# Performance work log

Measured on AMD Instinct MI355X. Metric: run time of the kernel, lower is better.

Reference implementation:

```python
import jax, jax.numpy as jnp
import numpy as np

B, L, D_NODE, D_EDGE, H = 4, 256, 256, 128, 8
DK = D_NODE // H        # 32, per-head node dim
DE = D_EDGE // H        # 16, per-head edge dim
NEG_SLOPE = 0.2

# Static index maps replicating the torch loop indexing (including its j-1 off-by-one / wraparound bug)
_GIDX = np.arange(L - 1)[None, :] + (np.arange(L - 1)[None, :] >= np.arange(L)[:, None])  # [L, L-1]: j-values visited for row i (j != i, in order)
_PIDX = (np.arange(L) - 1) % (L - 1)   # [L]: torch uses attention_probs[:, j-1] for every j != i
_II = np.arange(L)[:, None]            # [L, 1]


def lrelu(x):
    return jnp.where(x >= 0, x, NEG_SLOPE * x)


def setup_inputs() -> dict:
    key = jax.random.key(0)
    ks = jax.random.split(key, 19)
    w = lambda k, s, sc=0.05: jax.random.normal(k, s, jnp.float32) * sc
    return dict(
        node=w(ks[0], (B, L, D_NODE), 1.0),
        edge=w(ks[1], (B, L, L, D_EDGE), 1.0),
        Wn_w=w(ks[2], (D_NODE, D_NODE)), Wn_b=w(ks[3], (D_NODE,)),
        Wh_w=w(ks[4], (DK, DK)), Wh_b=w(ks[5], (DK,)),
        We_w=w(ks[6], (D_EDGE, D_EDGE)), We_b=w(ks[7], (D_EDGE,)),
        Wn2_w=w(ks[8], (D_NODE, D_NODE)), Wn2_b=w(ks[9], (D_NODE,)),
        We2_w=w(ks[10], (D_EDGE, D_EDGE)), We2_b=w(ks[11], (D_EDGE,)),
        attn_w=w(ks[12], (2 * DK + DE,)),                  # attn_linear (no bias), input order [hi, hj, eij]
        edge_w=w(ks[13], (DE + 2 * DK, DE)), edge_b=w(ks[14], (DE,)),  # edge_linear, input order [eij, hi, hj]
        out_n_w=w(ks[15], (D_NODE, D_NODE)), out_n_b=w(ks[16], (D_NODE,)),
        out_e_w=w(ks[17], (D_EDGE, D_EDGE)), out_e_b=w(ks[18], (D_EDGE,)),
    )


def reference(node, edge, Wn_w, Wn_b, Wh_w, Wh_b, We_w, We_b, Wn2_w, Wn2_b,
              We2_w, We2_b, attn_w, edge_w, edge_b, out_n_w, out_n_b, out_e_w, out_e_b):
    node_p = (node @ Wn_w + Wn_b).reshape(B, L, H, DK)
    edge_p = (edge @ We_w + We_b).reshape(B, L, L, H, DE)

    # ---- node update (all heads at once) ----
    wq, wk, we = attn_w[:DK], attn_w[DK:2 * DK], attn_w[2 * DK:]
    si = jnp.einsum('bihd,d->bih', node_p, wq)
    sj = jnp.einsum('bjhd,d->bjh', node_p, wk)
    se = jnp.einsum('bijhd,d->bijh', edge_p, we)
    scores = si[:, :, None, :] + sj[:, None, :, :] + se          # [B,L,L,H], score(i,j)
    sc = scores[:, _II, _GIDX, :]                                 # [B,L,L-1,H]: j != i, loop order
    probs = jax.nn.softmax(lrelu(sc), axis=2)                     # softmax over the L-1 neighbors
    probs_pair = probs[:, :, _PIDX, :]                            # [B,L,L,H]: replicate probs[:, j-1]
    mask = (1.0 - jnp.eye(L, dtype=node.dtype))[None, :, :, None]
    Whh = jnp.einsum('bjhd,de->bjhe', node_p, Wh_w) + Wh_b        # Wh(hj), bias inside the sum
    agg = jnp.einsum('bijh,bjhe->bihe', probs_pair * mask, Whh)
    node_h = (node_p + lrelu(agg)).reshape(B, L, D_NODE)          # concat heads == reshape
    new_node = node_h @ out_n_w + out_n_b

    # ---- edge update ----
    node_p2 = (new_node @ Wn2_w + Wn2_b).reshape(B, L, H, DK)
    edge_p2 = (edge @ We2_w + We2_b).reshape(B, L, L, H, DE)
    w_e, w_i, w_j = edge_w[:DE], edge_w[DE:DE + DK], edge_w[DE + DK:]
    e_new = (jnp.einsum('bijhd,de->bijhe', edge_p2, w_e)
             + jnp.einsum('bihd,de->bihe', node_p2, w_i)[:, :, None]
             + jnp.einsum('bjhd,de->bjhe', node_p2, w_j)[:, None]
             + edge_b)
    e_new = e_new * mask[..., None]                               # diagonal stays zero (zeros_like init)
    new_edge = e_new.reshape(B, L, L, D_EDGE) @ out_e_w + out_e_b
    return new_node, new_edge
```

## Files before the change

kernel.cpp:

```cpp
#include <hip/hip_runtime.h>

#define Bb 4
#define Ll 256
#define NEG 0.2f

typedef __attribute__((ext_vector_type(8))) short short8;
typedef __attribute__((ext_vector_type(4))) float f32x4;
typedef __attribute__((ext_vector_type(4))) unsigned uint4v;

__device__ __forceinline__ float lrelu(float x) { return x >= 0.f ? x : NEG * x; }

__device__ __forceinline__ short f2bf(float x) {
  unsigned u = __builtin_bit_cast(unsigned, x);
  unsigned r = (u + 0x7FFFu + ((u >> 16) & 1u)) >> 16;
  return (short)r;
}

__device__ __forceinline__ unsigned pack2bf(float e, float o) {
  unsigned ue = __builtin_bit_cast(unsigned, e);
  unsigned uo = __builtin_bit_cast(unsigned, o);
  return ((ue + 0x8000u) >> 16) | ((uo + 0x8000u) & 0xFFFF0000u);
}

__global__ void prep_kernel(const float* We_w, const float* We_b, const float* attn_w,
                            const float* We2_w, const float* We2_b, const float* edge_w,
                            const float* edge_b, const float* out_e_w, const float* out_e_b,
                            short* Vbf, float* chg, float* c0g, short* Gt) {
  int blk = blockIdx.x;
  int t = threadIdx.x;
  if (blk < 128) {
    __shared__ float m2[128];
    int c = blk;
    int h = t >> 4, e = t & 15;
    float s = 0.f;
    for (int d = 0; d < 16; ++d) s += We2_w[c * 128 + h * 16 + d] * edge_w[d * 16 + e];
    m2[t] = s;
    __syncthreads();
    float g = 0.f;
    for (int f = 0; f < 128; ++f) g += m2[f] * out_e_w[f * 128 + t];
    Gt[t * 128 + c] = f2bf(g);
  } else {
    __shared__ float b2e[128];
    const float* we = attn_w + 64;
    for (int idx = t; idx < 1024; idx += 128) {
      int c = idx >> 3, h = idx & 7;
      float s = 0.f;
      for (int d = 0; d < 16; ++d) s += We_w[c * 128 + h * 16 + d] * we[d];
      Vbf[h * 128 + c] = f2bf(s);
      Vbf[(h + 8) * 128 + c] = 0;
    }
    if (t < 8) {
      float s = 0.f;
      for (int d = 0; d < 16; ++d) s += We_b[t * 16 + d] * we[d];
      chg[t] = s;
    }
    {
      int h = t >> 4, e = t & 15;
      float s = 0.f;
      for (int d = 0; d < 16; ++d) s += We2_b[h * 16 + d] * edge_w[d * 16 + e];
      b2e[t] = s + edge_b[e];
    }
    __syncthreads();
    float s = out_e_b[t];
    for (int f = 0; f < 128; ++f) s += b2e[f] * out_e_w[f * 128 + t];
    c0g[t] = s;
  }
}

template <bool WE>
__global__ __launch_bounds__(256) void pass_a(const float* __restrict__ edge,
                                              const short* __restrict__ Vbf,
                                              const float* __restrict__ chg,
                                              short* __restrict__ ebf,
                                              float* __restrict__ seg) {
  int t = threadIdx.x;
  int l = t & 63, w = t >> 6;
  int lc = l & 15, lq = l >> 4;
  long slab = blockIdx.x;
  const float* ebase = edge + slab * 32768;

  short8 vb[4];
#pragma unroll
  for (int ks = 0; ks < 4; ++ks) vb[ks] = *(const short8*)(Vbf + lc * 128 + ks * 32 + lq * 8);

  f32x4 acc[4];
#pragma unroll
  for (int mf = 0; mf < 4; ++mf) acc[mf] = (f32x4){0.f, 0.f, 0.f, 0.f};

#pragma unroll
  for (int mf = 0; mf < 4; ++mf) {
    int row = w * 64 + mf * 16 + lc;
    const float* ap = ebase + row * 128 + lq * 8;
    float4 f[8];
#pragma unroll
    for (int ks = 0; ks < 4; ++ks) {
      f[2 * ks] = *(const float4*)(ap + ks * 32);
      f[2 * ks + 1] = *(const float4*)(ap + ks * 32 + 4);
    }
#pragma unroll
    for (int ks = 0; ks < 4; ++ks) {
      uint4v u;
      u.x = pack2bf(f[2 * ks].x, f[2 * ks].y);
      u.y = pack2bf(f[2 * ks].z, f[2 * ks].w);
      u.z = pack2bf(f[2 * ks + 1].x, f[2 * ks + 1].y);
      u.w = pack2bf(f[2 * ks + 1].z, f[2 * ks + 1].w);
      if constexpr (WE) *(uint4v*)(ebf + slab * 32768 + row * 128 + ks * 32 + lq * 8) = u;
      acc[mf] = __builtin_amdgcn_mfma_f32_16x16x32_bf16(vb[ks], __builtin_bit_cast(short8, u),
                                                        acc[mf], 0, 0, 0);
    }
  }
  if (lq < 2) {
    f32x4 chv = *(const f32x4*)(chg + lq * 4);
#pragma unroll
    for (int mf = 0; mf < 4; ++mf) {
      int row = w * 64 + mf * 16 + lc;
      f32x4 v = acc[mf] + chv;
      *(f32x4*)(seg + slab * 2048 + row * 8 + lq * 4) = v;
    }
  }
}

__global__ __launch_bounds__(256) void node_in_fused(
    const float* __restrict__ node, const float* __restrict__ Wn_w,
    const float* __restrict__ Wn_b, const float* __restrict__ Wh_w,
    const float* __restrict__ Wh_b, const float* __restrict__ attn_w,
    float* __restrict__ node_p, float* __restrict__ Whh, float* __restrict__ si,
    float* __restrict__ sj) {
  __shared__ float a[4][256];
  __shared__ float np[4][256];
  int t = threadIdx.x;
  int row0 = blockIdx.x * 4;
  for (int q = t; q < 1024; q += 256) a[q >> 8][q & 255] = node[(long)row0 * 256 + q];
  __syncthreads();
  float acc[4];
  float bvv = Wn_b[t];
#pragma unroll
  for (int r = 0; r < 4; ++r) acc[r] = bvv;
  for (int k = 0; k < 256; ++k) {
    float w = Wn_w[k * 256 + t];
#pragma unroll
    for (int r = 0; r < 4; ++r) acc[r] += a[r][k] * w;
  }
#pragma unroll
  for (int r = 0; r < 4; ++r) {
    node_p[(long)(row0 + r) * 256 + t] = acc[r];
    np[r][t] = acc[r];
  }
  __syncthreads();
  int h = t >> 5, e = t & 31;
  float wb2 = Wh_b[e];
#pragma unroll
  for (int r = 0; r < 4; ++r) {
    float s = wb2;
    for (int d = 0; d < 32; ++d) s += np[r][h * 32 + d] * Wh_w[d * 32 + e];
    Whh[(long)(row0 + r) * 256 + t] = s;
  }
  if (t < 64) {
    int r = t >> 4, idx = t & 15, hh = idx & 7;
    const float* w = attn_w + (idx < 8 ? 0 : 32);
    float s = 0.f;
    for (int d = 0; d < 32; ++d) s += np[r][hh * 32 + d] * w[d];
    ((idx < 8) ? si : sj)[(long)(row0 + r) * 8 + hh] = s;
  }
}

__global__ __launch_bounds__(256) void attn_fused(
    const float* __restrict__ node_p, const float* __restrict__ Whh,
    const float* __restrict__ si, const float* __restrict__ sj,
    const float* __restrict__ seg, float* __restrict__ node_h) {
  __shared__ float sjl[2048];
  __shared__ float sel[2048];
  __shared__ float pl[2048];
  __shared__ float sil[8];
  int t = threadIdx.x, bi = blockIdx.x;
  int b = bi >> 8, i = bi & 255;
  for (int q = t; q < 2048; q += 256) sjl[q] = sj[(long)b * 2048 + q];
  for (int q = t; q < 2048; q += 256) sel[q] = seg[(long)bi * 2048 + q];
  if (t < 8) sil[t] = si[(long)bi * 8 + t];
  __syncthreads();

  int g = t >> 5, l32 = t & 31;
  float sc[8];
  float mx = -1e30f;
#pragma unroll
  for (int m = 0; m < 8; ++m) {
    int k = l32 + 32 * m;
    float v = -1e30f;
    if (k < 255) {
      int jj = k + (k >= i ? 1 : 0);
      v = sil[g] + sjl[jj * 8 + g] + sel[jj * 8 + g];
      v = lrelu(v);
    }
    sc[m] = v;
    mx = fmaxf(mx, v);
  }
#pragma unroll
  for (int d = 16; d >= 1; d >>= 1) mx = fmaxf(mx, __shfl_xor(mx, d));
  float sum = 0.f;
#pragma unroll
  for (int m = 0; m < 8; ++m) {
    int k = l32 + 32 * m;
    float e = (k < 255) ? __expf(sc[m] - mx) : 0.f;
    sc[m] = e;
    sum += e;
  }
#pragma unroll
  for (int d = 16; d >= 1; d >>= 1) sum += __shfl_xor(sum, d);
  float inv = 1.f / sum;
#pragma unroll
  for (int m = 0; m < 8; ++m) {
    int k = l32 + 32 * m;
    if (k < 255) pl[k * 8 + g] = sc[m] * inv;
  }
  __syncthreads();

  int h = g;
  const float* wb = Whh + (long)b * 65536 + t;
  float acc0 = 0.f, acc1 = 0.f;
#pragma unroll 8
  for (int j = 0; j < 256; j += 2) {
    int k0 = (j == 0) ? 254 : (j - 1);
    int k1 = j;
    float w0 = (j == i) ? 0.f : pl[k0 * 8 + h];
    float w1 = (j + 1 == i) ? 0.f : pl[k1 * 8 + h];
    acc0 += w0 * wb[(long)j * 256];
    acc1 += w1 * wb[(long)(j + 1) * 256];
  }
  float acc = acc0 + acc1;
  float np = node_p[(long)bi * 256 + t];
  node_h[(long)bi * 256 + t] = np + lrelu(acc);
}

__global__ __launch_bounds__(256) void node_out_pq(
    const float* __restrict__ node_h, const float* __restrict__ out_n_w,
    const float* __restrict__ out_n_b, const float* __restrict__ Wn2_w,
    const float* __restrict__ Wn2_b, const float* __restrict__ edge_w,
    const float* __restrict__ out_e_w, float* __restrict__ out_node,
    float* __restrict__ Pg, float* __restrict__ Qg) {
  __shared__ float a[4][256];
  __shared__ float b2[4][256];
  __shared__ float ninj[4][256];
  int t = threadIdx.x;
  int row0 = blockIdx.x * 4;
  for (int q = t; q < 1024; q += 256) a[q >> 8][q & 255] = node_h[(long)row0 * 256 + q];
  __syncthreads();
  float acc[4];
  float bv1 = out_n_b[t];
#pragma unroll
  for (int r = 0; r < 4; ++r) acc[r] = bv1;
  for (int k = 0; k < 256; ++k) {
    float w = out_n_w[k * 256 + t];
#pragma unroll
    for (int r = 0; r < 4; ++r) acc[r] += a[r][k] * w;
  }
#pragma unroll
  for (int r = 0; r < 4; ++r) {
    out_node[(long)(row0 + r) * 256 + t] = acc[r];
    b2[r][t] = acc[r];
  }
  __syncthreads();
  float acc2[4];
  float bv2 = Wn2_b[t];
#pragma unroll
  for (int r = 0; r < 4; ++r) acc2[r] = bv2;
  for (int k = 0; k < 256; ++k) {
    float w = Wn2_w[k * 256 + t];
#pragma unroll
    for (int r = 0; r < 4; ++r) acc2[r] += b2[r][k] * w;
  }
#pragma unroll
  for (int r = 0; r < 4; ++r) a[r][t] = acc2[r];
  __syncthreads();
  {
    int f = t & 127, h = f >> 4, e = f & 15;
    const float* w = edge_w + 256 + (t >> 7) * 512;
#pragma unroll
    for (int r = 0; r < 4; ++r) {
      float s = 0.f;
      for (int d = 0; d < 32; ++d) s += a[r][h * 32 + d] * w[d * 16 + e];
      ninj[r][t] = s;
    }
  }
  __syncthreads();
  {
    int o = t & 127;
    int half = (t >> 7) * 128;
#pragma unroll
    for (int r = 0; r < 4; ++r) {
      float s = 0.f;
      const float* src = ninj[r] + half;
      for (int f = 0; f < 128; ++f) s += src[f] * out_e_w[f * 128 + o];
      ((t < 128) ? Pg : Qg)[(long)(row0 + r) * 128 + o] = s;
    }
  }
}

template <bool UE>
__global__ __launch_bounds__(256) void edge_out_kernel(
    const float* __restrict__ edge, const short* __restrict__ ebf,
    const short* __restrict__ Gt, const float* __restrict__ Pg,
    const float* __restrict__ Qg, const float* __restrict__ c0g,
    const float* __restrict__ oeb, float* __restrict__ out_edge) {
  int t = threadIdx.x;
  int l = t & 63, wid = t >> 6;
  int wm = wid >> 1, wn = wid & 1;
  int lc = l & 15, lq = l >> 4;

  long row0 = (long)blockIdx.x * 128;
  int b = (int)(row0 >> 16);
  int i = (int)((row0 >> 8) & 255);
  int j0 = (int)(row0 & 255);

  short8 bv[4][4];
#pragma unroll
  for (int ks = 0; ks < 4; ++ks)
#pragma unroll
    for (int nf = 0; nf < 4; ++nf)
      bv[ks][nf] = *(const short8*)(Gt + (wn * 64 + nf * 16 + lc) * 128 + ks * 32 + lq * 8);

  f32x4 acc[4][4];
#pragma unroll
  for (int mf = 0; mf < 4; ++mf)
#pragma unroll
    for (int nf = 0; nf < 4; ++nf) acc[mf][nf] = (f32x4){0.f, 0.f, 0.f, 0.f};

#pragma unroll
  for (int ks = 0; ks < 4; ++ks) {
    short8 av[4];
#pragma unroll
    for (int mf = 0; mf < 4; ++mf) {
      long row = row0 + wm * 64 + mf * 16 + lc;
      if constexpr (UE) {
        av[mf] = *(const short8*)(ebf + row * 128 + ks * 32 + lq * 8);
      } else {
        const float* ap = edge + row * 128 + ks * 32 + lq * 8;
        float4 f0 = *(const float4*)ap;
        float4 f1 = *(const float4*)(ap + 4);
        uint4v u;
        u.x = pack2bf(f0.x, f0.y);
        u.y = pack2bf(f0.z, f0.w);
        u.z = pack2bf(f1.x, f1.y);
        u.w = pack2bf(f1.z, f1.w);
        av[mf] = __builtin_bit_cast(short8, u);
      }
    }
#pragma unroll
    for (int mf = 0; mf < 4; ++mf)
#pragma unroll
      for (int nf = 0; nf < 4; ++nf)
        acc[mf][nf] =
            __builtin_amdgcn_mfma_f32_16x16x32_bf16(bv[ks][nf], av[mf], acc[mf][nf], 0, 0, 0);
  }

  f32x4 pc[4];
#pragma unroll
  for (int nf = 0; nf < 4; ++nf) {
    int cb = wn * 64 + nf * 16 + lq * 4;
    f32x4 p = *(const f32x4*)(Pg + ((long)(b * 256 + i)) * 128 + cb);
    f32x4 c0 = *(const f32x4*)(c0g + cb);
    pc[nf] = p + c0;
  }
#pragma unroll
  for (int mf = 0; mf < 4; ++mf) {
    int er = wm * 64 + mf * 16 + lc;
    int j = j0 + er;
    const float* Qrow = Qg + ((long)(b * 256 + j)) * 128;
    float* orow = out_edge + (row0 + er) * 128;
    if (j == i) {
#pragma unroll
      for (int nf = 0; nf < 4; ++nf) {
        int cb = wn * 64 + nf * 16 + lq * 4;
        *(f32x4*)(orow + cb) = *(const f32x4*)(oeb + cb);
      }
    } else {
#pragma unroll
      for (int nf = 0; nf < 4; ++nf) {
        int cb = wn * 64 + nf * 16 + lq * 4;
        f32x4 q4 = *(const f32x4*)(Qrow + cb);
        *(f32x4*)(orow + cb) = acc[mf][nf] + pc[nf] + q4;
      }
    }
  }
}

extern "C" void kernel_launch(void* const* d_in, const int* in_sizes, int n_in,
                              void* d_out, int out_size, void* d_ws, size_t ws_size,
                              hipStream_t stream) {
  const float* node = (const float*)d_in[0];
  const float* edge = (const float*)d_in[1];
  const float* Wn_w = (const float*)d_in[2];
  const float* Wn_b = (const float*)d_in[3];
  const float* Wh_w = (const float*)d_in[4];
  const float* Wh_b = (const float*)d_in[5];
  const float* We_w = (const float*)d_in[6];
  const float* We_b = (const float*)d_in[7];
  const float* Wn2_w = (const float*)d_in[8];
  const float* Wn2_b = (const float*)d_in[9];
  const float* We2_w = (const float*)d_in[10];
  const float* We2_b = (const float*)d_in[11];
  const float* attn_w = (const float*)d_in[12];
  const float* edge_w = (const float*)d_in[13];
  const float* edge_b = (const float*)d_in[14];
  const float* out_n_w = (const float*)d_in[15];
  const float* out_n_b = (const float*)d_in[16];
  const float* out_e_w = (const float*)d_in[17];
  const float* out_e_b = (const float*)d_in[18];

  float* out_node = (float*)d_out;
  float* out_edge = ((float*)d_out) + 262144;

  float* ws = (float*)d_ws;
  float* node_p = ws;
  float* Whh    = ws + 262144;
  float* node_h = ws + 524288;
  float* si     = ws + 786432;
  float* sjv    = ws + 794624;
  float* Pg     = ws + 802816;
  float* Qg     = ws + 933888;
  float* chg    = ws + 1064960;
  float* c0g    = ws + 1065088;
  short* Gt     = (short*)(ws + 1065216);
  short* Vbf    = (short*)(ws + 1073408);
  float* seg    = ws + 1074432;
  short* ebf    = (short*)(ws + 3171584);
  const bool big = ws_size >= (size_t)19948800 * 4;

  prep_kernel<<<129, 128, 0, stream>>>(We_w, We_b, attn_w, We2_w, We2_b, edge_w, edge_b,
                                       out_e_w, out_e_b, Vbf, chg, c0g, Gt);
  node_in_fused<<<256, 256, 0, stream>>>(node, Wn_w, Wn_b, Wh_w, Wh_b, attn_w, node_p, Whh,
                                         si, sjv);
  if (big)
    pass_a<true><<<1024, 256, 0, stream>>>(edge, Vbf, chg, ebf, seg);
  else
    pass_a<false><<<1024, 256, 0, stream>>>(edge, Vbf, chg, ebf, seg);
  attn_fused<<<1024, 256, 0, stream>>>(node_p, Whh, si, sjv, seg, node_h);
  node_out_pq<<<256, 256, 0, stream>>>(node_h, out_n_w, out_n_b, Wn2_w, Wn2_b, edge_w,
                                       out_e_w, out_node, Pg, Qg);
  if (big)
    edge_out_kernel<true><<<2048, 256, 0, stream>>>(edge, ebf, Gt, Pg, Qg, c0g, out_e_b,
                                                    out_edge);
  else
    edge_out_kernel<false><<<2048, 256, 0, stream>>>(edge, ebf, Gt, Pg, Qg, c0g, out_e_b,
                                                     out_edge);
}
```

Baseline: 193.5 us.

## Fuse edge-score MFMA into attention kernel and split bf16 packing pass

The pass_a kernel is removed. Its per-row edge score MFMA now runs inside attn_fused, which writes results straight to shared memory, so the seg buffer no longer makes a global round-trip. A separate streaming pack_kernel converts edge to bf16 for later reuse, and attn_fused reads that bf16 copy, which halves the edge bytes it reads. The edge-output stores become nontemporal to reduce cache pollution. In exchange there is an extra kernel launch, and attn_fused takes on more register and latency load.

```diff
diff --git a/kernel.cpp b/kernel.cpp
--- a/kernel.cpp
+++ b/kernel.cpp
@@ -67,56 +67,21 @@
   }
 }
 
-template <bool WE>
-__global__ __launch_bounds__(256) void pass_a(const float* __restrict__ edge,
-                                              const short* __restrict__ Vbf,
-                                              const float* __restrict__ chg,
-                                              short* __restrict__ ebf,
-                                              float* __restrict__ seg) {
-  int t = threadIdx.x;
-  int l = t & 63, w = t >> 6;
-  int lc = l & 15, lq = l >> 4;
-  long slab = blockIdx.x;
-  const float* ebase = edge + slab * 32768;
-
-  short8 vb[4];
-#pragma unroll
-  for (int ks = 0; ks < 4; ++ks) vb[ks] = *(const short8*)(Vbf + lc * 128 + ks * 32 + lq * 8);
-
-  f32x4 acc[4];
-#pragma unroll
-  for (int mf = 0; mf < 4; ++mf) acc[mf] = (f32x4){0.f, 0.f, 0.f, 0.f};
-
-#pragma unroll
-  for (int mf = 0; mf < 4; ++mf) {
-    int row = w * 64 + mf * 16 + lc;
-    const float* ap = ebase + row * 128 + lq * 8;
-    float4 f[8];
-#pragma unroll
-    for (int ks = 0; ks < 4; ++ks) {
-      f[2 * ks] = *(const float4*)(ap + ks * 32);
-      f[2 * ks + 1] = *(const float4*)(ap + ks * 32 + 4);
-    }
-#pragma unroll
-    for (int ks = 0; ks < 4; ++ks) {
-      uint4v u;
-      u.x = pack2bf(f[2 * ks].x, f[2 * ks].y);
-      u.y = pack2bf(f[2 * ks].z, f[2 * ks].w);
-      u.z = pack2bf(f[2 * ks + 1].x, f[2 * ks + 1].y);
-      u.w = pack2bf(f[2 * ks + 1].z, f[2 * ks + 1].w);
-      if constexpr (WE) *(uint4v*)(ebf + slab * 32768 + row * 128 + ks * 32 + lq * 8) = u;
-      acc[mf] = __builtin_amdgcn_mfma_f32_16x16x32_bf16(vb[ks], __builtin_bit_cast(short8, u),
-                                                        acc[mf], 0, 0, 0);
-    }
-  }
-  if (lq < 2) {
-    f32x4 chv = *(const f32x4*)(chg + lq * 4);
-#pragma unroll
-    for (int mf = 0; mf < 4; ++mf) {
-      int row = w * 64 + mf * 16 + lc;
-      f32x4 v = acc[mf] + chv;
-      *(f32x4*)(seg + slab * 2048 + row * 8 + lq * 4) = v;
-    }
+__global__ __launch_bounds__(256) void pack_kernel(const float* __restrict__ edge,
+                                                   short* __restrict__ ebf) {
+  long base = (long)blockIdx.x * 256 + threadIdx.x;
+#pragma unroll
+  for (int it = 0; it < 8; ++it) {
+    long g = base + (long)it * 524288;
+    const float4* src = reinterpret_cast<const float4*>(edge + g * 8);
+    float4 f0 = src[0];
+    float4 f1 = src[1];
+    uint4v u;
+    u.x = pack2bf(f0.x, f0.y);
+    u.y = pack2bf(f0.z, f0.w);
+    u.z = pack2bf(f1.x, f1.y);
+    u.w = pack2bf(f1.z, f1.w);
+    *(uint4v*)(ebf + g * 8) = u;
   }
 }
 
@@ -164,10 +129,13 @@
   }
 }
 
+template <bool UE>
 __global__ __launch_bounds__(256) void attn_fused(
     const float* __restrict__ node_p, const float* __restrict__ Whh,
     const float* __restrict__ si, const float* __restrict__ sj,
-    const float* __restrict__ seg, float* __restrict__ node_h) {
+    const short* __restrict__ ebf, const float* __restrict__ edge,
+    const short* __restrict__ Vbf, const float* __restrict__ chg,
+    float* __restrict__ node_h) {
   __shared__ float sjl[2048];
   __shared__ float sel[2048];
   __shared__ float pl[2048];
@@ -175,8 +143,49 @@
   int t = threadIdx.x, bi = blockIdx.x;
   int b = bi >> 8, i = bi & 255;
   for (int q = t; q < 2048; q += 256) sjl[q] = sj[(long)b * 2048 + q];
-  for (int q = t; q < 2048; q += 256) sel[q] = seg[(long)bi * 2048 + q];
   if (t < 8) sil[t] = si[(long)bi * 8 + t];
+
+  {
+    int l = t & 63, w = t >> 6;
+    int lc = l & 15, lq = l >> 4;
+    short8 vb[4];
+#pragma unroll
+    for (int ks = 0; ks < 4; ++ks) vb[ks] = *(const short8*)(Vbf + lc * 128 + ks * 32 + lq * 8);
+    f32x4 acc[4];
+#pragma unroll
+    for (int mf = 0; mf < 4; ++mf) acc[mf] = (f32x4){0.f, 0.f, 0.f, 0.f};
+#pragma unroll
+    for (int mf = 0; mf < 4; ++mf) {
+      int row = w * 64 + mf * 16 + lc;
+#pragma unroll
+      for (int ks = 0; ks < 4; ++ks) {
+        short8 av;
+        if constexpr (UE) {
+          av = *(const short8*)(ebf + (long)bi * 32768 + row * 128 + ks * 32 + lq * 8);
+        } else {
+          const float* ap = edge + (long)bi * 32768 + row * 128 + ks * 32 + lq * 8;
+          float4 f0 = *(const float4*)ap;
+          float4 f1 = *(const float4*)(ap + 4);
+          uint4v u;
+          u.x = pack2bf(f0.x, f0.y);
+          u.y = pack2bf(f0.z, f0.w);
+          u.z = pack2bf(f1.x, f1.y);
+          u.w = pack2bf(f1.z, f1.w);
+          av = __builtin_bit_cast(short8, u);
+        }
+        acc[mf] = __builtin_amdgcn_mfma_f32_16x16x32_bf16(vb[ks], av, acc[mf], 0, 0, 0);
+      }
+    }
+    if (lq < 2) {
+      f32x4 chv = *(const f32x4*)(chg + lq * 4);
+#pragma unroll
+      for (int mf = 0; mf < 4; ++mf) {
+        int row = w * 64 + mf * 16 + lc;
+        f32x4 v = acc[mf] + chv;
+        *(f32x4*)(&sel[row * 8 + lq * 4]) = v;
+      }
+    }
+  }
   __syncthreads();
 
   int g = t >> 5, l32 = t & 31;
@@ -370,14 +379,16 @@
 #pragma unroll
       for (int nf = 0; nf < 4; ++nf) {
         int cb = wn * 64 + nf * 16 + lq * 4;
-        *(f32x4*)(orow + cb) = *(const f32x4*)(oeb + cb);
+        f32x4 v = *(const f32x4*)(oeb + cb);
+        __builtin_nontemporal_store(v, (f32x4*)(orow + cb));
       }
     } else {
 #pragma unroll
       for (int nf = 0; nf < 4; ++nf) {
         int cb = wn * 64 + nf * 16 + lq * 4;
         f32x4 q4 = *(const f32x4*)(Qrow + cb);
-        *(f32x4*)(orow + cb) = acc[mf][nf] + pc[nf] + q4;
+        f32x4 v = acc[mf][nf] + pc[nf] + q4;
+        __builtin_nontemporal_store(v, (f32x4*)(orow + cb));
       }
     }
   }
@@ -421,19 +432,21 @@
   float* c0g    = ws + 1065088;
   short* Gt     = (short*)(ws + 1065216);
   short* Vbf    = (short*)(ws + 1073408);
-  float* seg    = ws + 1074432;
-  short* ebf    = (short*)(ws + 3171584);
-  const bool big = ws_size >= (size_t)19948800 * 4;
+  short* ebf    = (short*)(ws + 1074432);
+  const bool big = ws_size >= (size_t)(1074432 + 16777216) * 4;
 
   prep_kernel<<<129, 128, 0, stream>>>(We_w, We_b, attn_w, We2_w, We2_b, edge_w, edge_b,
                                        out_e_w, out_e_b, Vbf, chg, c0g, Gt);
   node_in_fused<<<256, 256, 0, stream>>>(node, Wn_w, Wn_b, Wh_w, Wh_b, attn_w, node_p, Whh,
                                          si, sjv);
-  if (big)
-    pass_a<true><<<1024, 256, 0, stream>>>(edge, Vbf, chg, ebf, seg);
-  else
-    pass_a<false><<<1024, 256, 0, stream>>>(edge, Vbf, chg, ebf, seg);
-  attn_fused<<<1024, 256, 0, stream>>>(node_p, Whh, si, sjv, seg, node_h);
+  if (big) {
+    pack_kernel<<<2048, 256, 0, stream>>>(edge, ebf);
+    attn_fused<true><<<1024, 256, 0, stream>>>(node_p, Whh, si, sjv, ebf, edge, Vbf, chg,
+                                               node_h);
+  } else {
+    attn_fused<false><<<1024, 256, 0, stream>>>(node_p, Whh, si, sjv, ebf, edge, Vbf, chg,
+                                                node_h);
+  }
   node_out_pq<<<256, 256, 0, stream>>>(node_h, out_n_w, out_n_b, Wn2_w, Wn2_b, edge_w,
                                        out_e_w, out_node, Pg, Qg);
   if (big)
```

Result: faster. 171.0 us (-11.6%).

## Drop bf16 edge cache, stage swizzled G in LDS, retile edge output kernel

Applied to the files above, without the earlier changes.

Removes the intermediate bf16 copy of the edge tensor (ebf) that pass_a wrote and edge_out re-read. The edge output kernel now re-reads fp32 edge directly and converts on the fly. The G weight matrix is stored pre-swizzled so each block can stage it in shared memory without bank conflicts. Each block now handles a whole (b,i) slab with 8 column fragments per wave, and the score kernel is split into smaller blocks. This trades one bf16 write plus read for a second fp32 read of edge. The output stores become scalar per-lane writes instead of float4, which may hurt write coalescing.

```diff
diff --git a/kernel.cpp b/kernel.cpp
--- a/kernel.cpp
+++ b/kernel.cpp
@@ -25,7 +25,7 @@
 __global__ void prep_kernel(const float* We_w, const float* We_b, const float* attn_w,
                             const float* We2_w, const float* We2_b, const float* edge_w,
                             const float* edge_b, const float* out_e_w, const float* out_e_b,
-                            short* Vbf, float* chg, float* c0g, short* Gt) {
+                            short* Vbf, float* chg, float* c0g, short* Gsw) {
   int blk = blockIdx.x;
   int t = threadIdx.x;
   if (blk < 128) {
@@ -38,7 +38,8 @@
     __syncthreads();
     float g = 0.f;
     for (int f = 0; f < 128; ++f) g += m2[f] * out_e_w[f * 128 + t];
-    Gt[t * 128 + c] = f2bf(g);
+    int off = t * 256 + ((2 * c) ^ ((t & 7) << 4));
+    *(short*)((char*)Gsw + off) = f2bf(g);
   } else {
     __shared__ float b2e[128];
     const float* we = attn_w + 64;
@@ -67,55 +68,45 @@
   }
 }
 
-template <bool WE>
-__global__ __launch_bounds__(256) void pass_a(const float* __restrict__ edge,
-                                              const short* __restrict__ Vbf,
-                                              const float* __restrict__ chg,
-                                              short* __restrict__ ebf,
-                                              float* __restrict__ seg) {
+__global__ __launch_bounds__(256) void se_kernel(const float* __restrict__ edge,
+                                                 const short* __restrict__ Vbf,
+                                                 const float* __restrict__ chg,
+                                                 float* __restrict__ seg) {
   int t = threadIdx.x;
-  int l = t & 63, w = t >> 6;
+  int w = t >> 6, l = t & 63;
   int lc = l & 15, lq = l >> 4;
-  long slab = blockIdx.x;
-  const float* ebase = edge + slab * 32768;
-
+  int blk = blockIdx.x;
+  long rbase = (long)blk * 128;
   short8 vb[4];
 #pragma unroll
   for (int ks = 0; ks < 4; ++ks) vb[ks] = *(const short8*)(Vbf + lc * 128 + ks * 32 + lq * 8);
-
-  f32x4 acc[4];
-#pragma unroll
-  for (int mf = 0; mf < 4; ++mf) acc[mf] = (f32x4){0.f, 0.f, 0.f, 0.f};
-
-#pragma unroll
-  for (int mf = 0; mf < 4; ++mf) {
-    int row = w * 64 + mf * 16 + lc;
-    const float* ap = ebase + row * 128 + lq * 8;
-    float4 f[8];
+  float chv = (lc < 8) ? chg[lc] : 0.f;
+  int slab = blk >> 1;
+  int joff = (blk & 1) * 128;
+
+#pragma unroll
+  for (int s = 0; s < 2; ++s) {
+    int rowb = w * 32 + s * 16;
+    f32x4 acc = (f32x4){0.f, 0.f, 0.f, 0.f};
 #pragma unroll
     for (int ks = 0; ks < 4; ++ks) {
-      f[2 * ks] = *(const float4*)(ap + ks * 32);
-      f[2 * ks + 1] = *(const float4*)(ap + ks * 32 + 4);
-    }
-#pragma unroll
-    for (int ks = 0; ks < 4; ++ks) {
+      const float* ap = edge + (rbase + rowb + lc) * 128 + ks * 32 + lq * 8;
+      float4 f0 = *(const float4*)ap;
+      float4 f1 = *(const float4*)(ap + 4);
       uint4v u;
-      u.x = pack2bf(f[2 * ks].x, f[2 * ks].y);
-      u.y = pack2bf(f[2 * ks].z, f[2 * ks].w);
-      u.z = pack2bf(f[2 * ks + 1].x, f[2 * ks + 1].y);
-      u.w = pack2bf(f[2 * ks + 1].z, f[2 * ks + 1].w);
-      if constexpr (WE) *(uint4v*)(ebf + slab * 32768 + row * 128 + ks * 32 + lq * 8) = u;
-      acc[mf] = __builtin_amdgcn_mfma_f32_16x16x32_bf16(vb[ks], __builtin_bit_cast(short8, u),
-                                                        acc[mf], 0, 0, 0);
-    }
-  }
-  if (lq < 2) {
-    f32x4 chv = *(const f32x4*)(chg + lq * 4);
-#pragma unroll
-    for (int mf = 0; mf < 4; ++mf) {
-      int row = w * 64 + mf * 16 + lc;
-      f32x4 v = acc[mf] + chv;
-      *(f32x4*)(seg + slab * 2048 + row * 8 + lq * 4) = v;
+      u.x = pack2bf(f0.x, f0.y);
+      u.y = pack2bf(f0.z, f0.w);
+      u.z = pack2bf(f1.x, f1.y);
+      u.w = pack2bf(f1.z, f1.w);
+      acc = __builtin_amdgcn_mfma_f32_16x16x32_bf16(__builtin_bit_cast(short8, u), vb[ks], acc,
+                                                    0, 0, 0);
+    }
+    if (lc < 8) {
+#pragma unroll
+      for (int r = 0; r < 4; ++r) {
+        int row = joff + rowb + lq * 4 + r;
+        seg[(long)slab * 2048 + row * 8 + lc] = acc[r] + chv;
+      }
     }
   }
 }
@@ -295,89 +286,70 @@
   }
 }
 
-template <bool UE>
 __global__ __launch_bounds__(256) void edge_out_kernel(
-    const float* __restrict__ edge, const short* __restrict__ ebf,
-    const short* __restrict__ Gt, const float* __restrict__ Pg,
-    const float* __restrict__ Qg, const float* __restrict__ c0g,
-    const float* __restrict__ oeb, float* __restrict__ out_edge) {
+    const float* __restrict__ edge, const short* __restrict__ Gsw,
+    const float* __restrict__ Pg, const float* __restrict__ Qg,
+    const float* __restrict__ c0g, const float* __restrict__ oeb,
+    float* __restrict__ out_edge) {
+  __shared__ __align__(16) char Gl[32768];
   int t = threadIdx.x;
-  int l = t & 63, wid = t >> 6;
-  int wm = wid >> 1, wn = wid & 1;
+  int w = t >> 6, l = t & 63;
   int lc = l & 15, lq = l >> 4;
-
-  long row0 = (long)blockIdx.x * 128;
-  int b = (int)(row0 >> 16);
-  int i = (int)((row0 >> 8) & 255);
-  int j0 = (int)(row0 & 255);
-
-  short8 bv[4][4];
-#pragma unroll
-  for (int ks = 0; ks < 4; ++ks)
-#pragma unroll
-    for (int nf = 0; nf < 4; ++nf)
-      bv[ks][nf] = *(const short8*)(Gt + (wn * 64 + nf * 16 + lc) * 128 + ks * 32 + lq * 8);
-
-  f32x4 acc[4][4];
-#pragma unroll
-  for (int mf = 0; mf < 4; ++mf)
-#pragma unroll
-    for (int nf = 0; nf < 4; ++nf) acc[mf][nf] = (f32x4){0.f, 0.f, 0.f, 0.f};
-
-#pragma unroll
-  for (int ks = 0; ks < 4; ++ks) {
-    short8 av[4];
-#pragma unroll
-    for (int mf = 0; mf < 4; ++mf) {
-      long row = row0 + wm * 64 + mf * 16 + lc;
-      if constexpr (UE) {
-        av[mf] = *(const short8*)(ebf + row * 128 + ks * 32 + lq * 8);
-      } else {
-        const float* ap = edge + row * 128 + ks * 32 + lq * 8;
-        float4 f0 = *(const float4*)ap;
-        float4 f1 = *(const float4*)(ap + 4);
-        uint4v u;
-        u.x = pack2bf(f0.x, f0.y);
-        u.y = pack2bf(f0.z, f0.w);
-        u.z = pack2bf(f1.x, f1.y);
-        u.w = pack2bf(f1.z, f1.w);
-        av[mf] = __builtin_bit_cast(short8, u);
+  int bi = blockIdx.x;
+  int b = bi >> 8, i = bi & 255;
+
+  {
+    const uint4v* gsrc = (const uint4v*)Gsw;
+    uint4v* gdst = (uint4v*)Gl;
+#pragma unroll
+    for (int q = 0; q < 8; ++q) gdst[q * 256 + t] = gsrc[q * 256 + t];
+  }
+  float pcv[8], oebv[8];
+#pragma unroll
+  for (int nf = 0; nf < 8; ++nf) {
+    int col = nf * 16 + lc;
+    pcv[nf] = Pg[(long)bi * 128 + col] + c0g[col];
+    oebv[nf] = oeb[col];
+  }
+  __syncthreads();
+
+  const float* eslab = edge + (long)bi * 32768;
+#pragma unroll
+  for (int s = 0; s < 4; ++s) {
+    int rowb = w * 64 + s * 16;
+    f32x4 acc[8];
+#pragma unroll
+    for (int nf = 0; nf < 8; ++nf) acc[nf] = (f32x4){0.f, 0.f, 0.f, 0.f};
+#pragma unroll
+    for (int ks = 0; ks < 4; ++ks) {
+      const float* ap = eslab + (long)(rowb + lc) * 128 + ks * 32 + lq * 8;
+      float4 f0 = *(const float4*)ap;
+      float4 f1 = *(const float4*)(ap + 4);
+      uint4v u;
+      u.x = pack2bf(f0.x, f0.y);
+      u.y = pack2bf(f0.z, f0.w);
+      u.z = pack2bf(f1.x, f1.y);
+      u.w = pack2bf(f1.z, f1.w);
+      short8 av = __builtin_bit_cast(short8, u);
+#pragma unroll
+      for (int nf = 0; nf < 8; ++nf) {
+        int col = nf * 16 + lc;
+        short8 bvv =
+            *(const short8*)(Gl + col * 256 + ((ks * 64 + lq * 16) ^ ((col & 7) << 4)));
+        acc[nf] = __builtin_amdgcn_mfma_f32_16x16x32_bf16(av, bvv, acc[nf], 0, 0, 0);
       }
     }
 #pragma unroll
-    for (int mf = 0; mf < 4; ++mf)
-#pragma unroll
-      for (int nf = 0; nf < 4; ++nf)
-        acc[mf][nf] =
-            __builtin_amdgcn_mfma_f32_16x16x32_bf16(bv[ks][nf], av[mf], acc[mf][nf], 0, 0, 0);
-  }
-
-  f32x4 pc[4];
-#pragma unroll
-  for (int nf = 0; nf < 4; ++nf) {
-    int cb = wn * 64 + nf * 16 + lq * 4;
-    f32x4 p = *(const f32x4*)(Pg + ((long)(b * 256 + i)) * 128 + cb);
-    f32x4 c0 = *(const f32x4*)(c0g + cb);
-    pc[nf] = p + c0;
-  }
-#pragma unroll
-  for (int mf = 0; mf < 4; ++mf) {
-    int er = wm * 64 + mf * 16 + lc;
-    int j = j0 + er;
-    const float* Qrow = Qg + ((long)(b * 256 + j)) * 128;
-    float* orow = out_edge + (row0 + er) * 128;
-    if (j == i) {
-#pragma unroll
-      for (int nf = 0; nf < 4; ++nf) {
-        int cb = wn * 64 + nf * 16 + lq * 4;
-        *(f32x4*)(orow + cb) = *(const f32x4*)(oeb + cb);
-      }
-    } else {
-#pragma unroll
-      for (int nf = 0; nf < 4; ++nf) {
-        int cb = wn * 64 + nf * 16 + lq * 4;
-        f32x4 q4 = *(const f32x4*)(Qrow + cb);
-        *(f32x4*)(orow + cb) = acc[mf][nf] + pc[nf] + q4;
+    for (int r = 0; r < 4; ++r) {
+      int jloc = rowb + lq * 4 + r;
+      float* orow = out_edge + ((long)bi * 256 + jloc) * 128;
+      const float* Qrow = Qg + (long)(b * 256 + jloc) * 128;
+      bool diag = (jloc == i);
+#pragma unroll
+      for (int nf = 0; nf < 8; ++nf) {
+        int col = nf * 16 + lc;
+        float v = diag ? oebv[nf] : (acc[nf][r] + pcv[nf] + Qrow[col]);
+        orow[col] = v;
       }
     }
   }
@@ -419,27 +391,17 @@
   float* Qg     = ws + 933888;
   float* chg    = ws + 1064960;
   float* c0g    = ws + 1065088;
-  short* Gt     = (short*)(ws + 1065216);
+  short* Gsw    = (short*)(ws + 1065216);
   short* Vbf    = (short*)(ws + 1073408);
   float* seg    = ws + 1074432;
-  short* ebf    = (short*)(ws + 3171584);
-  const bool big = ws_size >= (size_t)19948800 * 4;
 
   prep_kernel<<<129, 128, 0, stream>>>(We_w, We_b, attn_w, We2_w, We2_b, edge_w, edge_b,
-                                       out_e_w, out_e_b, Vbf, chg, c0g, Gt);
+                                       out_e_w, out_e_b, Vbf, chg, c0g, Gsw);
   node_in_fused<<<256, 256, 0, stream>>>(node, Wn_w, Wn_b, Wh_w, Wh_b, attn_w, node_p, Whh,
                                          si, sjv);
-  if (big)
-    pass_a<true><<<1024, 256, 0, stream>>>(edge, Vbf, chg, ebf, seg);
-  else
-    pass_a<false><<<1024, 256, 0, stream>>>(edge, Vbf, chg, ebf, seg);
+  se_kernel<<<2048, 256, 0, stream>>>(edge, Vbf, chg, seg);
   attn_fused<<<1024, 256, 0, stream>>>(node_p, Whh, si, sjv, seg, node_h);
   node_out_pq<<<256, 256, 0, stream>>>(node_h, out_n_w, out_n_b, Wn2_w, Wn2_b, edge_w,
                                        out_e_w, out_node, Pg, Qg);
-  if (big)
-    edge_out_kernel<true><<<2048, 256, 0, stream>>>(edge, ebf, Gt, Pg, Qg, c0g, out_e_b,
-                                                    out_edge);
-  else
-    edge_out_kernel<false><<<2048, 256, 0, stream>>>(edge, ebf, Gt, Pg, Qg, c0g, out_e_b,
-                                                     out_edge);
-}
+  edge_out_kernel<<<1024, 256, 0, stream>>>(edge, Gsw, Pg, Qg, c0g, out_e_b, out_edge);
+}
```

Result: faster. 170.9 us (-11.7%).
